# Performance work log

Measured on AMD Instinct MI355X. Metric: run time of the kernel, lower is better.

Reference implementation:

```python
import jax, jax.numpy as jnp
import numpy as np

NEG = -1e6

def setup_inputs() -> dict:
    key = jax.random.key(0)
    ks = jax.random.split(key, 7)
    B, Q, K, H, Dv = 16, 64, 1024, 256, 256
    return {
        "queries": jax.random.normal(ks[0], (B, Q, H), jnp.float32),
        "keys": jax.random.normal(ks[1], (B, K, H), jnp.float32),
        "values": jax.random.normal(ks[2], (B, K, Dv), jnp.float32),
        "valid_lens": jax.random.randint(ks[3], (B,), 1, K + 1),
        "Wq": jax.random.normal(ks[4], (H, H), jnp.float32) / np.sqrt(H),
        "Wk": jax.random.normal(ks[5], (H, H), jnp.float32) / np.sqrt(H),
        "wv": jax.random.normal(ks[6], (H,), jnp.float32) / np.sqrt(H),
    }

def reference(queries, keys, values, valid_lens, Wq, Wk, wv):
    # projections: [B,Q,H], [B,K,H]
    q = jnp.einsum("bqd,hd->bqh", queries, Wq)
    k = jnp.einsum("bkd,hd->bkh", keys, Wk)
    # broadcast add + tanh: [B,Q,K,H]
    features = jnp.tanh(q[:, :, None, :] + k[:, None, :, :])
    # score reduction over hidden: [B,Q,K]
    scores = jnp.einsum("bqkh,h->bqk", features, wv)
    # masked softmax over the key axis (1D valid_lens per batch)
    K = keys.shape[1]
    mask = jnp.arange(K)[None, None, :] < valid_lens[:, None, None]  # [B,1,K]
    scores = jnp.where(mask, scores, NEG)
    attn = jax.nn.softmax(scores, axis=-1)
    # weighted sum over values: [B,Q,Dv]
    return jnp.einsum("bqk,bkv->bqv", attn, values)
```

## Files before the change

### kernel.cpp

```cpp
#include <hip/hip_runtime.h>

#define LOG2E 1.4426950408889634f
#define TANH_SCALE 2.8853900817779268f
#define NEG_BIG -1e30f

typedef __attribute__((ext_vector_type(8))) short bf16x8;
typedef __attribute__((ext_vector_type(4))) float f32x4;

static __device__ __forceinline__ short f2bf(float f) {
    unsigned u = __builtin_bit_cast(unsigned, f);
    u += 0x7fffu + ((u >> 16) & 1u);
    return (short)(u >> 16);
}

__global__ __launch_bounds__(256) void proj_mfma(const float* __restrict__ queries,
                                                 const float* __restrict__ keys,
                                                 const float* __restrict__ Wq,
                                                 const float* __restrict__ Wk,
                                                 float* __restrict__ eq,
                                                 float* __restrict__ ek) {
    __shared__ char As[64 * 128];
    __shared__ char Bs[128 * 128];

    const int mtile = blockIdx.x;
    const float* A; const float* W; float* dst; int m0;
    if (mtile < 16) { A = queries; W = Wq; dst = eq; m0 = mtile << 6; }
    else            { A = keys;    W = Wk; dst = ek; m0 = (mtile - 16) << 6; }

    const int tid = threadIdx.x;
    const int w = tid >> 6, lane = tid & 63;
    const int wm = w >> 1, wn = w & 1;
    const int n0 = blockIdx.y << 7;
    const int r = lane & 15, kq = lane >> 4;

    f32x4 acc[2][4] = {};

    const int ra = tid >> 2, sa = tid & 3;
    const int rb = tid >> 1, hb = tid & 1;

    for (int ks = 0; ks < 4; ++ks) {
        const int k0 = ks << 6;
        __syncthreads();
        {
            const float* srcA = &A[(m0 + ra) * 256 + k0 + (sa << 4)];
            #pragma unroll
            for (int g = 0; g < 2; ++g) {
                float4 f0 = *reinterpret_cast<const float4*>(srcA + (g << 3));
                float4 f1 = *reinterpret_cast<const float4*>(srcA + (g << 3) + 4);
                bf16x8 pk = {f2bf(f0.x), f2bf(f0.y), f2bf(f0.z), f2bf(f0.w),
                             f2bf(f1.x), f2bf(f1.y), f2bf(f1.z), f2bf(f1.w)};
                int byt = (ra << 7) + (((sa << 5) + (g << 4)) ^ ((ra & 7) << 4));
                *reinterpret_cast<bf16x8*>(As + byt) = pk;
            }
            const float* srcB = &W[(n0 + rb) * 256 + k0 + (hb << 5)];
            #pragma unroll
            for (int g = 0; g < 4; ++g) {
                float4 f0 = *reinterpret_cast<const float4*>(srcB + (g << 3));
                float4 f1 = *reinterpret_cast<const float4*>(srcB + (g << 3) + 4);
                bf16x8 pk = {f2bf(f0.x), f2bf(f0.y), f2bf(f0.z), f2bf(f0.w),
                             f2bf(f1.x), f2bf(f1.y), f2bf(f1.z), f2bf(f1.w)};
                int byt = (rb << 7) + (((hb << 6) + (g << 4)) ^ ((rb & 7) << 4));
                *reinterpret_cast<bf16x8*>(Bs + byt) = pk;
            }
        }
        __syncthreads();

        bf16x8 af[2][2], bfr[4][2];
        #pragma unroll
        for (int kf = 0; kf < 2; ++kf) {
            #pragma unroll
            for (int mi = 0; mi < 2; ++mi) {
                int row = (wm << 5) + (mi << 4) + r;
                int byt = (row << 7) + (((kf << 6) + (kq << 4)) ^ ((row & 7) << 4));
                af[mi][kf] = *reinterpret_cast<const bf16x8*>(As + byt);
            }
            #pragma unroll
            for (int nj = 0; nj < 4; ++nj) {
                int row = (wn << 6) + (nj << 4) + r;
                int byt = (row << 7) + (((kf << 6) + (kq << 4)) ^ ((row & 7) << 4));
                bfr[nj][kf] = *reinterpret_cast<const bf16x8*>(Bs + byt);
            }
        }
        #pragma unroll
        for (int kf = 0; kf < 2; ++kf)
            #pragma unroll
            for (int mi = 0; mi < 2; ++mi)
                #pragma unroll
                for (int nj = 0; nj < 4; ++nj)
                    acc[mi][nj] = __builtin_amdgcn_mfma_f32_16x16x32_bf16(
                        af[mi][kf], bfr[nj][kf], acc[mi][nj], 0, 0, 0);
    }

    #pragma unroll
    for (int mi = 0; mi < 2; ++mi)
        #pragma unroll
        for (int nj = 0; nj < 4; ++nj)
            #pragma unroll
            for (int t = 0; t < 4; ++t) {
                int row = m0 + (wm << 5) + (mi << 4) + (kq << 2) + t;
                int col = n0 + (wn << 6) + (nj << 4) + r;
                dst[row * 256 + col] = __builtin_amdgcn_exp2f(TANH_SCALE * acc[mi][nj][t]);
            }
}

__global__ __launch_bounds__(256) void attn_kernel(const float* __restrict__ eq,
                                                   const float* __restrict__ ek,
                                                   const float* __restrict__ values,
                                                   const int* __restrict__ valid_lens,
                                                   const float* __restrict__ wv,
                                                   float* __restrict__ part_acc,
                                                   float* __restrict__ part_m,
                                                   float* __restrict__ part_l) {
    __shared__ float4 ek_lds[64 * 32];
    __shared__ float p_lds[8][64];

    const int tid = threadIdx.x;
    const int w = tid >> 6, lane = tid & 63;
    const int qt = blockIdx.x, b = blockIdx.y, seg = blockIdx.z;
    const int q0 = (qt << 3) + (w << 1);
    const int vl = valid_lens[b];
    const int kstart = seg << 7;
    const int pidx0 = (((b << 6) + q0) << 3) + seg;

    if (kstart >= vl) {
        f32x4 z = {0.f, 0.f, 0.f, 0.f};
        *reinterpret_cast<f32x4*>(&part_acc[(size_t)pidx0 * 256 + (lane << 2)]) = z;
        *reinterpret_cast<f32x4*>(&part_acc[(size_t)(pidx0 + 8) * 256 + (lane << 2)]) = z;
        if (lane == 0) {
            part_m[pidx0] = NEG_BIG;     part_l[pidx0] = 0.f;
            part_m[pidx0 + 8] = NEG_BIG; part_l[pidx0 + 8] = 0.f;
        }
        return;
    }

    const float4* eq0 = reinterpret_cast<const float4*>(&eq[((b << 6) + q0) * 256]);
    const float4* eq1 = reinterpret_cast<const float4*>(&eq[((b << 6) + q0 + 1) * 256]);
    const float4* wv4 = reinterpret_cast<const float4*>(wv);

    const int kend = min(kstart + 128, vl);
    const int nchunks = (kend - kstart + 63) >> 6;

    float mA = -INFINITY, lA = 0.f, mB = -INFINITY, lB = 0.f;
    f32x4 accA = {0.f, 0.f, 0.f, 0.f}, accB = {0.f, 0.f, 0.f, 0.f};

    const int krow = lane << 5;
    const int ksw = lane & 7;

    for (int c = 0; c < nchunks; ++c) {
        const int ck = kstart + (c << 6);
        float s0 = 0.f, s1 = 0.f;

        #pragma unroll
        for (int half = 0; half < 2; ++half) {
            __syncthreads();
            {
                const float4* src =
                    reinterpret_cast<const float4*>(&ek[(size_t)(b * 1024 + ck) * 256]) + (half << 5);
                #pragma unroll
                for (int i = 0; i < 8; ++i) {
                    int d = (i << 8) + tid;
                    int row = d >> 5, col = d & 31;
                    ek_lds[(row << 5) + (col ^ (row & 7))] = src[row * 64 + col];
                }
            }
            __syncthreads();

            const int hoff = half << 5;
            #pragma unroll 8
            for (int jh = 0; jh < 32; ++jh) {
                float4 kv = ek_lds[krow + (jh ^ ksw)];
                float4 qa = eq0[hoff + jh];
                float4 qb = eq1[hoff + jh];
                float4 wc = wv4[hoff + jh];
                s0 += wc.x * __builtin_amdgcn_rcpf(fmaf(kv.x, qa.x, 1.0f));
                s0 += wc.y * __builtin_amdgcn_rcpf(fmaf(kv.y, qa.y, 1.0f));
                s0 += wc.z * __builtin_amdgcn_rcpf(fmaf(kv.z, qa.z, 1.0f));
                s0 += wc.w * __builtin_amdgcn_rcpf(fmaf(kv.w, qa.w, 1.0f));
                s1 += wc.x * __builtin_amdgcn_rcpf(fmaf(kv.x, qb.x, 1.0f));
                s1 += wc.y * __builtin_amdgcn_rcpf(fmaf(kv.y, qb.y, 1.0f));
                s1 += wc.z * __builtin_amdgcn_rcpf(fmaf(kv.z, qb.z, 1.0f));
                s1 += wc.w * __builtin_amdgcn_rcpf(fmaf(kv.w, qb.w, 1.0f));
            }
        }
        float sA = -2.0f * s0;
        float sB = -2.0f * s1;
        if (ck + lane >= vl) { sA = NEG_BIG; sB = NEG_BIG; }

        float mcA = sA, mcB = sB;
        #pragma unroll
        for (int o = 32; o > 0; o >>= 1) {
            mcA = fmaxf(mcA, __shfl_xor(mcA, o));
            mcB = fmaxf(mcB, __shfl_xor(mcB, o));
        }
        float mnA = fmaxf(mA, mcA), mnB = fmaxf(mB, mcB);
        float rA = __builtin_amdgcn_exp2f((mA - mnA) * LOG2E);
        float rB = __builtin_amdgcn_exp2f((mB - mnB) * LOG2E);
        float pA = __builtin_amdgcn_exp2f((sA - mnA) * LOG2E);
        float pB = __builtin_amdgcn_exp2f((sB - mnB) * LOG2E);
        float lcA = pA, lcB = pB;
        #pragma unroll
        for (int o = 32; o > 0; o >>= 1) {
            lcA += __shfl_xor(lcA, o);
            lcB += __shfl_xor(lcB, o);
        }
        lA = lA * rA + lcA; mA = mnA;
        lB = lB * rB + lcB; mB = mnB;
        accA *= rA; accB *= rB;
        p_lds[(w << 1) + 0][lane] = pA;
        p_lds[(w << 1) + 1][lane] = pB;

        const int nv = min(64, kend - ck);
        const float* vsrc = &values[(size_t)(b * 1024 + ck) * 256 + (lane << 2)];
        if (nv == 64) {
            #pragma unroll 8
            for (int j = 0; j < 64; ++j) {
                float pa = p_lds[(w << 1)][j], pb = p_lds[(w << 1) + 1][j];
                float4 v = *reinterpret_cast<const float4*>(vsrc + j * 256);
                accA.x += pa * v.x; accA.y += pa * v.y; accA.z += pa * v.z; accA.w += pa * v.w;
                accB.x += pb * v.x; accB.y += pb * v.y; accB.z += pb * v.z; accB.w += pb * v.w;
            }
        } else {
            for (int j = 0; j < nv; ++j) {
                float pa = p_lds[(w << 1)][j], pb = p_lds[(w << 1) + 1][j];
                float4 v = *reinterpret_cast<const float4*>(vsrc + j * 256);
                accA.x += pa * v.x; accA.y += pa * v.y; accA.z += pa * v.z; accA.w += pa * v.w;
                accB.x += pb * v.x; accB.y += pb * v.y; accB.z += pb * v.z; accB.w += pb * v.w;
            }
        }
    }

    if (lane == 0) {
        part_m[pidx0] = mA;     part_l[pidx0] = lA;
        part_m[pidx0 + 8] = mB; part_l[pidx0 + 8] = lB;
    }
    *reinterpret_cast<f32x4*>(&part_acc[(size_t)pidx0 * 256 + (lane << 2)]) = accA;
    *reinterpret_cast<f32x4*>(&part_acc[(size_t)(pidx0 + 8) * 256 + (lane << 2)]) = accB;
}

__global__ __launch_bounds__(256) void combine_kernel(const float* __restrict__ part_acc,
                                                      const float* __restrict__ part_m,
                                                      const float* __restrict__ part_l,
                                                      float* __restrict__ out) {
    const int tid = threadIdx.x;
    const int w = tid >> 6, lane = tid & 63;
    const int b = blockIdx.x >> 4, qt = blockIdx.x & 15;
    const int q = (qt << 2) + w;
    const int base = (((b << 6) + q) << 3);

    float mm[8], ll[8];
    #pragma unroll
    for (int i = 0; i < 8; ++i) { mm[i] = part_m[base + i]; ll[i] = part_l[base + i]; }
    float M = mm[0];
    #pragma unroll
    for (int i = 1; i < 8; ++i) M = fmaxf(M, mm[i]);
    float wt[8];
    float L = 0.f;
    #pragma unroll
    for (int i = 0; i < 8; ++i) {
        wt[i] = __builtin_amdgcn_exp2f((mm[i] - M) * LOG2E);
        L += wt[i] * ll[i];
    }
    float invL = 1.0f / L;
    float4 o = {0.f, 0.f, 0.f, 0.f};
    #pragma unroll
    for (int i = 0; i < 8; ++i) {
        float4 v = *reinterpret_cast<const float4*>(&part_acc[(size_t)(base + i) * 256 + (lane << 2)]);
        o.x += wt[i] * v.x; o.y += wt[i] * v.y; o.z += wt[i] * v.z; o.w += wt[i] * v.w;
    }
    o.x *= invL; o.y *= invL; o.z *= invL; o.w *= invL;
    *reinterpret_cast<float4*>(&out[((b << 6) + q) * 256 + (lane << 2)]) = o;
}

extern "C" void kernel_launch(void* const* d_in, const int* in_sizes, int n_in,
                              void* d_out, int out_size, void* d_ws, size_t ws_size,
                              hipStream_t stream) {
    const float* queries    = (const float*)d_in[0];
    const float* keys       = (const float*)d_in[1];
    const float* values     = (const float*)d_in[2];
    const int*   valid_lens = (const int*)d_in[3];
    const float* Wq         = (const float*)d_in[4];
    const float* Wk         = (const float*)d_in[5];
    const float* wv         = (const float*)d_in[6];
    float* out = (float*)d_out;

    float* eqw      = (float*)d_ws;
    float* ekw      = eqw + 262144;
    float* part_acc = ekw + 4194304;
    float* part_m   = part_acc + 2097152;
    float* part_l   = part_m + 8192;

    proj_mfma<<<dim3(272, 2), 256, 0, stream>>>(queries, keys, Wq, Wk, eqw, ekw);
    attn_kernel<<<dim3(8, 16, 8), 256, 0, stream>>>(eqw, ekw, values, valid_lens, wv,
                                                    part_acc, part_m, part_l);
    combine_kernel<<<dim3(256), 256, 0, stream>>>(part_acc, part_m, part_l, out);
}
```

Measured before the change: 162.9 us.

## Register-prefetch key tiles, stage queries/wv in LDS, fp16 partials, LDS-free projection

The projection kernel drops its LDS staging and loads bf16 fragments straight from global memory, using smaller 32-row tiles and writing into one combined buffer. The attention kernel prefetches the next half-chunk of projected keys and queries into registers while computing the current one, and stages queries and wv in LDS instead of reading them from global memory. Partial accumulators are stored as fp16 to halve the traffic into the combine kernel, and p values are read as float4. The risks are extra register pressure from the prefetch buffers, fp16 precision loss in the partials, and redundant global loads of W in the projection.

```diff
diff --git a/kernel.cpp b/kernel.cpp
--- a/kernel.cpp
+++ b/kernel.cpp
@@ -6,6 +6,7 @@
 
 typedef __attribute__((ext_vector_type(8))) short bf16x8;
 typedef __attribute__((ext_vector_type(4))) float f32x4;
+typedef _Float16 half4 __attribute__((ext_vector_type(4)));
 
 static __device__ __forceinline__ short f2bf(float f) {
     unsigned u = __builtin_bit_cast(unsigned, f);
@@ -17,176 +18,161 @@
                                                  const float* __restrict__ keys,
                                                  const float* __restrict__ Wq,
                                                  const float* __restrict__ Wk,
-                                                 float* __restrict__ eq,
-                                                 float* __restrict__ ek) {
-    __shared__ char As[64 * 128];
-    __shared__ char Bs[128 * 128];
-
-    const int mtile = blockIdx.x;
-    const float* A; const float* W; float* dst; int m0;
-    if (mtile < 16) { A = queries; W = Wq; dst = eq; m0 = mtile << 6; }
-    else            { A = keys;    W = Wk; dst = ek; m0 = (mtile - 16) << 6; }
-
+                                                 float* __restrict__ e_all) {
+    const int mt = blockIdx.x >> 1, nt = blockIdx.x & 1;
     const int tid = threadIdx.x;
     const int w = tid >> 6, lane = tid & 63;
     const int wm = w >> 1, wn = w & 1;
-    const int n0 = blockIdx.y << 7;
     const int r = lane & 15, kq = lane >> 4;
-
-    f32x4 acc[2][4] = {};
-
-    const int ra = tid >> 2, sa = tid & 3;
-    const int rb = tid >> 1, hb = tid & 1;
-
-    for (int ks = 0; ks < 4; ++ks) {
-        const int k0 = ks << 6;
-        __syncthreads();
-        {
-            const float* srcA = &A[(m0 + ra) * 256 + k0 + (sa << 4)];
-            #pragma unroll
-            for (int g = 0; g < 2; ++g) {
-                float4 f0 = *reinterpret_cast<const float4*>(srcA + (g << 3));
-                float4 f1 = *reinterpret_cast<const float4*>(srcA + (g << 3) + 4);
-                bf16x8 pk = {f2bf(f0.x), f2bf(f0.y), f2bf(f0.z), f2bf(f0.w),
-                             f2bf(f1.x), f2bf(f1.y), f2bf(f1.z), f2bf(f1.w)};
-                int byt = (ra << 7) + (((sa << 5) + (g << 4)) ^ ((ra & 7) << 4));
-                *reinterpret_cast<bf16x8*>(As + byt) = pk;
-            }
-            const float* srcB = &W[(n0 + rb) * 256 + k0 + (hb << 5)];
-            #pragma unroll
-            for (int g = 0; g < 4; ++g) {
-                float4 f0 = *reinterpret_cast<const float4*>(srcB + (g << 3));
-                float4 f1 = *reinterpret_cast<const float4*>(srcB + (g << 3) + 4);
-                bf16x8 pk = {f2bf(f0.x), f2bf(f0.y), f2bf(f0.z), f2bf(f0.w),
-                             f2bf(f1.x), f2bf(f1.y), f2bf(f1.z), f2bf(f1.w)};
-                int byt = (rb << 7) + (((hb << 6) + (g << 4)) ^ ((rb & 7) << 4));
-                *reinterpret_cast<bf16x8*>(Bs + byt) = pk;
-            }
-        }
-        __syncthreads();
-
-        bf16x8 af[2][2], bfr[4][2];
-        #pragma unroll
-        for (int kf = 0; kf < 2; ++kf) {
-            #pragma unroll
-            for (int mi = 0; mi < 2; ++mi) {
-                int row = (wm << 5) + (mi << 4) + r;
-                int byt = (row << 7) + (((kf << 6) + (kq << 4)) ^ ((row & 7) << 4));
-                af[mi][kf] = *reinterpret_cast<const bf16x8*>(As + byt);
-            }
-            #pragma unroll
-            for (int nj = 0; nj < 4; ++nj) {
-                int row = (wn << 6) + (nj << 4) + r;
-                int byt = (row << 7) + (((kf << 6) + (kq << 4)) ^ ((row & 7) << 4));
-                bfr[nj][kf] = *reinterpret_cast<const bf16x8*>(Bs + byt);
-            }
-        }
-        #pragma unroll
-        for (int kf = 0; kf < 2; ++kf)
-            #pragma unroll
-            for (int mi = 0; mi < 2; ++mi)
-                #pragma unroll
-                for (int nj = 0; nj < 4; ++nj)
-                    acc[mi][nj] = __builtin_amdgcn_mfma_f32_16x16x32_bf16(
-                        af[mi][kf], bfr[nj][kf], acc[mi][nj], 0, 0, 0);
-    }
-
-    #pragma unroll
-    for (int mi = 0; mi < 2; ++mi)
-        #pragma unroll
-        for (int nj = 0; nj < 4; ++nj)
-            #pragma unroll
-            for (int t = 0; t < 4; ++t) {
-                int row = m0 + (wm << 5) + (mi << 4) + (kq << 2) + t;
-                int col = n0 + (wn << 6) + (nj << 4) + r;
-                dst[row * 256 + col] = __builtin_amdgcn_exp2f(TANH_SCALE * acc[mi][nj][t]);
-            }
-}
-
-__global__ __launch_bounds__(256) void attn_kernel(const float* __restrict__ eq,
-                                                   const float* __restrict__ ek,
-                                                   const float* __restrict__ values,
-                                                   const int* __restrict__ valid_lens,
-                                                   const float* __restrict__ wv,
-                                                   float* __restrict__ part_acc,
-                                                   float* __restrict__ part_m,
-                                                   float* __restrict__ part_l) {
+    const int m0 = mt << 5;
+    const int ncol = (nt << 7) + (wn << 6);
+
+    const float* A; const float* W; int ar;
+    if (m0 < 1024) { A = queries; W = Wq; ar = m0; }
+    else           { A = keys;    W = Wk; ar = m0 - 1024; }
+
+    const float* aptr = &A[(size_t)(ar + (wm << 4) + r) * 256];
+    f32x4 acc[4] = {};
+
+    #pragma unroll 2
+    for (int ks = 0; ks < 8; ++ks) {
+        const int k0 = (ks << 5) + (kq << 3);
+        float4 fa0 = *reinterpret_cast<const float4*>(aptr + k0);
+        float4 fa1 = *reinterpret_cast<const float4*>(aptr + k0 + 4);
+        bf16x8 a = {f2bf(fa0.x), f2bf(fa0.y), f2bf(fa0.z), f2bf(fa0.w),
+                    f2bf(fa1.x), f2bf(fa1.y), f2bf(fa1.z), f2bf(fa1.w)};
+        #pragma unroll
+        for (int nj = 0; nj < 4; ++nj) {
+            const float* bp = &W[(size_t)(ncol + (nj << 4) + r) * 256 + k0];
+            float4 fb0 = *reinterpret_cast<const float4*>(bp);
+            float4 fb1 = *reinterpret_cast<const float4*>(bp + 4);
+            bf16x8 bb = {f2bf(fb0.x), f2bf(fb0.y), f2bf(fb0.z), f2bf(fb0.w),
+                         f2bf(fb1.x), f2bf(fb1.y), f2bf(fb1.z), f2bf(fb1.w)};
+            acc[nj] = __builtin_amdgcn_mfma_f32_16x16x32_bf16(a, bb, acc[nj], 0, 0, 0);
+        }
+    }
+    #pragma unroll
+    for (int nj = 0; nj < 4; ++nj)
+        #pragma unroll
+        for (int t = 0; t < 4; ++t) {
+            int row = m0 + (wm << 4) + (kq << 2) + t;
+            e_all[(size_t)row * 256 + ncol + (nj << 4) + r] =
+                __builtin_amdgcn_exp2f(TANH_SCALE * acc[nj][t]);
+        }
+}
+
+#define ATTN_ISSUE(RS, RQ, STG) do {                                           \
+    const float4* src_ = ekb + (((STG) >> 1) << 12) + (((STG) & 1) << 5);      \
+    _Pragma("unroll")                                                          \
+    for (int i_ = 0; i_ < 8; ++i_) {                                           \
+        int d_ = (i_ << 8) + tid;                                              \
+        RS[i_] = src_[(d_ >> 5) * 64 + (d_ & 31)];                             \
+    }                                                                          \
+    RQ = eqf[(size_t)((b << 6) + q0 + (tid >> 5)) * 64                         \
+             + (((STG) & 1) << 5) + (tid & 31)];                               \
+} while (0)
+
+#define ATTN_WRITE(RS, RQ) do {                                                \
+    _Pragma("unroll")                                                          \
+    for (int i_ = 0; i_ < 8; ++i_) {                                           \
+        int d_ = (i_ << 8) + tid;                                              \
+        int row_ = d_ >> 5, col_ = d_ & 31;                                    \
+        ek_lds[(row_ << 5) + (col_ ^ (row_ & 7))] = RS[i_];                    \
+    }                                                                          \
+    q_lds[tid] = RQ;                                                           \
+} while (0)
+
+#define ATTN_COMPUTE(S0, S1, HOFF) do {                                        \
+    _Pragma("unroll 8")                                                        \
+    for (int jh = 0; jh < 32; ++jh) {                                          \
+        float4 kv = ek_lds[krow + (jh ^ ksw)];                                 \
+        float4 qa = q_lds[qoff + jh];                                          \
+        float4 qb = q_lds[qoff + 32 + jh];                                     \
+        float4 wc = wv_lds[(HOFF) + jh];                                       \
+        S0 += wc.x * __builtin_amdgcn_rcpf(fmaf(kv.x, qa.x, 1.0f));            \
+        S0 += wc.y * __builtin_amdgcn_rcpf(fmaf(kv.y, qa.y, 1.0f));            \
+        S0 += wc.z * __builtin_amdgcn_rcpf(fmaf(kv.z, qa.z, 1.0f));            \
+        S0 += wc.w * __builtin_amdgcn_rcpf(fmaf(kv.w, qa.w, 1.0f));            \
+        S1 += wc.x * __builtin_amdgcn_rcpf(fmaf(kv.x, qb.x, 1.0f));            \
+        S1 += wc.y * __builtin_amdgcn_rcpf(fmaf(kv.y, qb.y, 1.0f));            \
+        S1 += wc.z * __builtin_amdgcn_rcpf(fmaf(kv.z, qb.z, 1.0f));            \
+        S1 += wc.w * __builtin_amdgcn_rcpf(fmaf(kv.w, qb.w, 1.0f));            \
+    }                                                                          \
+} while (0)
+
+__global__ __launch_bounds__(256, 4) void attn_kernel(const float* __restrict__ e_all,
+                                                      const float* __restrict__ values,
+                                                      const int* __restrict__ valid_lens,
+                                                      const float* __restrict__ wv,
+                                                      _Float16* __restrict__ part_acc,
+                                                      float* __restrict__ part_m,
+                                                      float* __restrict__ part_l) {
     __shared__ float4 ek_lds[64 * 32];
-    __shared__ float p_lds[8][64];
+    __shared__ float4 q_lds[256];
+    __shared__ float4 wv_lds[64];
+    __shared__ float  p_lds[8][64];
 
     const int tid = threadIdx.x;
     const int w = tid >> 6, lane = tid & 63;
     const int qt = blockIdx.x, b = blockIdx.y, seg = blockIdx.z;
-    const int q0 = (qt << 3) + (w << 1);
+    const int q0 = qt << 3;
     const int vl = valid_lens[b];
     const int kstart = seg << 7;
-    const int pidx0 = (((b << 6) + q0) << 3) + seg;
+    const int pA = (((b << 6) + q0 + (w << 1)) << 3) + seg;
+    const int pB = pA + 8;
 
     if (kstart >= vl) {
-        f32x4 z = {0.f, 0.f, 0.f, 0.f};
-        *reinterpret_cast<f32x4*>(&part_acc[(size_t)pidx0 * 256 + (lane << 2)]) = z;
-        *reinterpret_cast<f32x4*>(&part_acc[(size_t)(pidx0 + 8) * 256 + (lane << 2)]) = z;
+        half4 z = {};
+        *reinterpret_cast<half4*>(&part_acc[(size_t)pA * 256 + (lane << 2)]) = z;
+        *reinterpret_cast<half4*>(&part_acc[(size_t)pB * 256 + (lane << 2)]) = z;
         if (lane == 0) {
-            part_m[pidx0] = NEG_BIG;     part_l[pidx0] = 0.f;
-            part_m[pidx0 + 8] = NEG_BIG; part_l[pidx0 + 8] = 0.f;
+            part_m[pA] = NEG_BIG; part_l[pA] = 0.f;
+            part_m[pB] = NEG_BIG; part_l[pB] = 0.f;
         }
         return;
     }
-
-    const float4* eq0 = reinterpret_cast<const float4*>(&eq[((b << 6) + q0) * 256]);
-    const float4* eq1 = reinterpret_cast<const float4*>(&eq[((b << 6) + q0 + 1) * 256]);
-    const float4* wv4 = reinterpret_cast<const float4*>(wv);
 
     const int kend = min(kstart + 128, vl);
     const int nchunks = (kend - kstart + 63) >> 6;
+    const int nst = nchunks << 1;
+
+    const float4* ekb = reinterpret_cast<const float4*>(&e_all[(size_t)(1024 + b * 1024 + kstart) * 256]);
+    const float4* eqf = reinterpret_cast<const float4*>(e_all);
+    const float4* wvf = reinterpret_cast<const float4*>(wv);
+
+    if (tid < 64) wv_lds[tid] = wvf[tid];
+
+    const int krow = lane << 5;
+    const int ksw  = lane & 7;
+    const int qoff = w << 6;
 
     float mA = -INFINITY, lA = 0.f, mB = -INFINITY, lB = 0.f;
     f32x4 accA = {0.f, 0.f, 0.f, 0.f}, accB = {0.f, 0.f, 0.f, 0.f};
 
-    const int krow = lane << 5;
-    const int ksw = lane & 7;
+    float4 rsA[8], rsB[8];
+    float4 rqA, rqB;
+
+    ATTN_ISSUE(rsA, rqA, 0);
 
     for (int c = 0; c < nchunks; ++c) {
         const int ck = kstart + (c << 6);
         float s0 = 0.f, s1 = 0.f;
 
-        #pragma unroll
-        for (int half = 0; half < 2; ++half) {
-            __syncthreads();
-            {
-                const float4* src =
-                    reinterpret_cast<const float4*>(&ek[(size_t)(b * 1024 + ck) * 256]) + (half << 5);
-                #pragma unroll
-                for (int i = 0; i < 8; ++i) {
-                    int d = (i << 8) + tid;
-                    int row = d >> 5, col = d & 31;
-                    ek_lds[(row << 5) + (col ^ (row & 7))] = src[row * 64 + col];
-                }
-            }
-            __syncthreads();
-
-            const int hoff = half << 5;
-            #pragma unroll 8
-            for (int jh = 0; jh < 32; ++jh) {
-                float4 kv = ek_lds[krow + (jh ^ ksw)];
-                float4 qa = eq0[hoff + jh];
-                float4 qb = eq1[hoff + jh];
-                float4 wc = wv4[hoff + jh];
-                s0 += wc.x * __builtin_amdgcn_rcpf(fmaf(kv.x, qa.x, 1.0f));
-                s0 += wc.y * __builtin_amdgcn_rcpf(fmaf(kv.y, qa.y, 1.0f));
-                s0 += wc.z * __builtin_amdgcn_rcpf(fmaf(kv.z, qa.z, 1.0f));
-                s0 += wc.w * __builtin_amdgcn_rcpf(fmaf(kv.w, qa.w, 1.0f));
-                s1 += wc.x * __builtin_amdgcn_rcpf(fmaf(kv.x, qb.x, 1.0f));
-                s1 += wc.y * __builtin_amdgcn_rcpf(fmaf(kv.y, qb.y, 1.0f));
-                s1 += wc.z * __builtin_amdgcn_rcpf(fmaf(kv.z, qb.z, 1.0f));
-                s1 += wc.w * __builtin_amdgcn_rcpf(fmaf(kv.w, qb.w, 1.0f));
-            }
-        }
-        float sA = -2.0f * s0;
-        float sB = -2.0f * s1;
-        if (ck + lane >= vl) { sA = NEG_BIG; sB = NEG_BIG; }
-
-        float mcA = sA, mcB = sB;
+        __syncthreads();
+        ATTN_WRITE(rsA, rqA);
+        __syncthreads();
+        ATTN_ISSUE(rsB, rqB, (c << 1) + 1);
+        ATTN_COMPUTE(s0, s1, 0);
+
+        __syncthreads();
+        ATTN_WRITE(rsB, rqB);
+        __syncthreads();
+        if ((c << 1) + 2 < nst) ATTN_ISSUE(rsA, rqA, (c << 1) + 2);
+        ATTN_COMPUTE(s0, s1, 32);
+
+        float sA_ = -2.0f * s0, sB_ = -2.0f * s1;
+        if (ck + lane >= vl) { sA_ = NEG_BIG; sB_ = NEG_BIG; }
+        float mcA = sA_, mcB = sB_;
         #pragma unroll
         for (int o = 32; o > 0; o >>= 1) {
             mcA = fmaxf(mcA, __shfl_xor(mcA, o));
@@ -195,9 +181,9 @@
         float mnA = fmaxf(mA, mcA), mnB = fmaxf(mB, mcB);
         float rA = __builtin_amdgcn_exp2f((mA - mnA) * LOG2E);
         float rB = __builtin_amdgcn_exp2f((mB - mnB) * LOG2E);
-        float pA = __builtin_amdgcn_exp2f((sA - mnA) * LOG2E);
-        float pB = __builtin_amdgcn_exp2f((sB - mnB) * LOG2E);
-        float lcA = pA, lcB = pB;
+        float pA_ = __builtin_amdgcn_exp2f((sA_ - mnA) * LOG2E);
+        float pB_ = __builtin_amdgcn_exp2f((sB_ - mnB) * LOG2E);
+        float lcA = pA_, lcB = pB_;
         #pragma unroll
         for (int o = 32; o > 0; o >>= 1) {
             lcA += __shfl_xor(lcA, o);
@@ -206,18 +192,23 @@
         lA = lA * rA + lcA; mA = mnA;
         lB = lB * rB + lcB; mB = mnB;
         accA *= rA; accB *= rB;
-        p_lds[(w << 1) + 0][lane] = pA;
-        p_lds[(w << 1) + 1][lane] = pB;
+        p_lds[(w << 1) + 0][lane] = pA_;
+        p_lds[(w << 1) + 1][lane] = pB_;
 
         const int nv = min(64, kend - ck);
         const float* vsrc = &values[(size_t)(b * 1024 + ck) * 256 + (lane << 2)];
         if (nv == 64) {
-            #pragma unroll 8
-            for (int j = 0; j < 64; ++j) {
-                float pa = p_lds[(w << 1)][j], pb = p_lds[(w << 1) + 1][j];
-                float4 v = *reinterpret_cast<const float4*>(vsrc + j * 256);
-                accA.x += pa * v.x; accA.y += pa * v.y; accA.z += pa * v.z; accA.w += pa * v.w;
-                accB.x += pb * v.x; accB.y += pb * v.y; accB.z += pb * v.z; accB.w += pb * v.w;
+            #pragma unroll 4
+            for (int j4 = 0; j4 < 16; ++j4) {
+                float4 pa4 = *reinterpret_cast<const float4*>(&p_lds[(w << 1)][j4 << 2]);
+                float4 pb4 = *reinterpret_cast<const float4*>(&p_lds[(w << 1) + 1][j4 << 2]);
+                #pragma unroll
+                for (int jj = 0; jj < 4; ++jj) {
+                    float pa = ((const float*)&pa4)[jj], pb = ((const float*)&pb4)[jj];
+                    float4 v = *reinterpret_cast<const float4*>(vsrc + (((j4 << 2) + jj)) * 256);
+                    accA.x += pa * v.x; accA.y += pa * v.y; accA.z += pa * v.z; accA.w += pa * v.w;
+                    accB.x += pb * v.x; accB.y += pb * v.y; accB.z += pb * v.z; accB.w += pb * v.w;
+                }
             }
         } else {
             for (int j = 0; j < nv; ++j) {
@@ -230,14 +221,16 @@
     }
 
     if (lane == 0) {
-        part_m[pidx0] = mA;     part_l[pidx0] = lA;
-        part_m[pidx0 + 8] = mB; part_l[pidx0 + 8] = lB;
-    }
-    *reinterpret_cast<f32x4*>(&part_acc[(size_t)pidx0 * 256 + (lane << 2)]) = accA;
-    *reinterpret_cast<f32x4*>(&part_acc[(size_t)(pidx0 + 8) * 256 + (lane << 2)]) = accB;
-}
-
-__global__ __launch_bounds__(256) void combine_kernel(const float* __restrict__ part_acc,
+        part_m[pA] = mA; part_l[pA] = lA;
+        part_m[pB] = mB; part_l[pB] = lB;
+    }
+    half4 ha = {(_Float16)accA.x, (_Float16)accA.y, (_Float16)accA.z, (_Float16)accA.w};
+    half4 hb = {(_Float16)accB.x, (_Float16)accB.y, (_Float16)accB.z, (_Float16)accB.w};
+    *reinterpret_cast<half4*>(&part_acc[(size_t)pA * 256 + (lane << 2)]) = ha;
+    *reinterpret_cast<half4*>(&part_acc[(size_t)pB * 256 + (lane << 2)]) = hb;
+}
+
+__global__ __launch_bounds__(256) void combine_kernel(const _Float16* __restrict__ part_acc,
                                                       const float* __restrict__ part_m,
                                                       const float* __restrict__ part_l,
                                                       float* __restrict__ out) {
@@ -245,7 +238,7 @@
     const int w = tid >> 6, lane = tid & 63;
     const int b = blockIdx.x >> 4, qt = blockIdx.x & 15;
     const int q = (qt << 2) + w;
-    const int base = (((b << 6) + q) << 3);
+    const int base = ((b << 6) + q) << 3;
 
     float mm[8], ll[8];
     #pragma unroll
@@ -264,11 +257,12 @@
     float4 o = {0.f, 0.f, 0.f, 0.f};
     #pragma unroll
     for (int i = 0; i < 8; ++i) {
-        float4 v = *reinterpret_cast<const float4*>(&part_acc[(size_t)(base + i) * 256 + (lane << 2)]);
-        o.x += wt[i] * v.x; o.y += wt[i] * v.y; o.z += wt[i] * v.z; o.w += wt[i] * v.w;
+        half4 v = *reinterpret_cast<const half4*>(&part_acc[(size_t)(base + i) * 256 + (lane << 2)]);
+        o.x += wt[i] * (float)v.x; o.y += wt[i] * (float)v.y;
+        o.z += wt[i] * (float)v.z; o.w += wt[i] * (float)v.w;
     }
     o.x *= invL; o.y *= invL; o.z *= invL; o.w *= invL;
-    *reinterpret_cast<float4*>(&out[((b << 6) + q) * 256 + (lane << 2)]) = o;
+    *reinterpret_cast<float4*>(&out[(size_t)((b << 6) + q) * 256 + (lane << 2)]) = o;
 }
 
 extern "C" void kernel_launch(void* const* d_in, const int* in_sizes, int n_in,
@@ -283,14 +277,13 @@
     const float* wv         = (const float*)d_in[6];
     float* out = (float*)d_out;
 
-    float* eqw      = (float*)d_ws;
-    float* ekw      = eqw + 262144;
-    float* part_acc = ekw + 4194304;
-    float* part_m   = part_acc + 2097152;
-    float* part_l   = part_m + 8192;
-
-    proj_mfma<<<dim3(272, 2), 256, 0, stream>>>(queries, keys, Wq, Wk, eqw, ekw);
-    attn_kernel<<<dim3(8, 16, 8), 256, 0, stream>>>(eqw, ekw, values, valid_lens, wv,
+    float*     e_all    = (float*)d_ws;
+    _Float16*  part_acc = (_Float16*)(e_all + 4456448);
+    float*     part_m   = (float*)(part_acc + 2097152);
+    float*     part_l   = part_m + 8192;
+
+    proj_mfma<<<dim3(1088), 256, 0, stream>>>(queries, keys, Wq, Wk, e_all);
+    attn_kernel<<<dim3(8, 16, 8), 256, 0, stream>>>(e_all, values, valid_lens, wv,
                                                     part_acc, part_m, part_l);
     combine_kernel<<<dim3(256), 256, 0, stream>>>(part_acc, part_m, part_l, out);
 }
```

New measurement: 215.5 us. 1.32x slower.
